# Performance work log

Hardware: AMD Instinct MI355X
Metric: run time of the kernel (lower is better)

## Reference

```python
import jax, jax.numpy as jnp
import numpy as np

B, L, C, R = 4, 2048, 16, 16
A_SCALE = 0.05  # keep spectral radius of transition matrices < 1 over L=2048 steps


def setup_inputs() -> dict:
    key = jax.random.key(0)
    k1, k2 = jax.random.split(key)
    A = jax.random.normal(k1, (B, L, C, R, R), dtype=jnp.float32) * A_SCALE
    X = jax.random.normal(k2, (B, L, C, R, R), dtype=jnp.float32)
    return {"A": A, "X": X}


def reference(A, X):
    # Linear matrix recurrence: Y_t = A_t @ Y_{t-1} + X_t (Y_0 = X_0),
    # computed in log-depth via an associative scan over the time axis (L).
    # Combine rule matches the Triton scan_combine_matrix:
    #   a_new = a_curr @ a_prev;  x_new = a_curr @ x_prev + x_curr
    def combine(e1, e2):
        a1, x1 = e1  # earlier segment
        a2, x2 = e2  # later segment
        a = jnp.einsum('blcik,blckj->blcij', a2, a1)
        x = jnp.einsum('blcik,blckj->blcij', a2, x1) + x2
        return (a, x)

    _, Y = jax.lax.associative_scan(combine, (A, X), axis=1)
    return Y  # [B, L, C, R, R]
```

## Files before the change

### kernel.cpp

```cpp
#include <hip/hip_runtime.h>

constexpr int B = 4, L = 2048, C = 16, R = 16;
constexpr int M = R * R;
constexpr int G = 64;
constexpr int S = L / G;
constexpr int T = 4;

__device__ __forceinline__ long mat_off(int b, int l, int c) {
    return (((long)b * L + l) * C + c) * M;
}

__global__ __launch_bounds__(256) void pass1_chunk_agg(
    const float* __restrict__ A, const float* __restrict__ X,
    float* __restrict__ ws) {
    const int blk = blockIdx.x;
    const int g   = blk % G;
    const int bc  = blk / G;
    const int b   = bc / C, c = bc % C;
    const int tid = threadIdx.x;
    const int i = tid >> 4, j = tid & 15;

    __shared__ float sA[T][M];
    __shared__ float sX[T][M];
    __shared__ float aggA[M];
    __shared__ float aggX[M];

    aggA[tid] = (i == j) ? 1.0f : 0.0f;
    aggX[tid] = 0.0f;

    const int tm = tid >> 6;
    const int e4 = (tid & 63) << 2;

    for (int t0 = 0; t0 < S; t0 += T) {
        const int l = g * S + t0 + tm;
        const float4 va = *(const float4*)(A + mat_off(b, l, c) + e4);
        const float4 vx = *(const float4*)(X + mat_off(b, l, c) + e4);
        *(float4*)&sA[tm][e4] = va;
        *(float4*)&sX[tm][e4] = vx;
        __syncthreads();
        for (int s = 0; s < T; ++s) {
            float accA = 0.0f;
            float accX = sX[s][tid];
            #pragma unroll
            for (int k = 0; k < 16; ++k) {
                const float a = sA[s][(i << 4) + k];
                accA += a * aggA[(k << 4) + j];
                accX += a * aggX[(k << 4) + j];
            }
            __syncthreads();
            aggA[tid] = accA;
            aggX[tid] = accX;
            __syncthreads();
        }
    }
    float* slot = ws + (long)blk * (2 * M);
    slot[tid]     = aggA[tid];
    slot[M + tid] = aggX[tid];
}

__global__ __launch_bounds__(256) void pass2_scan(float* __restrict__ ws) {
    const int bc  = blockIdx.x;
    const int tid = threadIdx.x;
    const int i = tid >> 4, j = tid & 15;

    __shared__ float sAg[M];
    __shared__ float carry[M];
    carry[tid] = 0.0f;

    float* base = ws + (long)bc * G * (2 * M);
    for (int g = 0; g < G; ++g) {
        float* slot = base + (long)g * (2 * M);
        sAg[tid] = slot[tid];
        const float xg  = slot[M + tid];
        const float old = carry[tid];
        __syncthreads();
        float acc = xg;
        #pragma unroll
        for (int k = 0; k < 16; ++k)
            acc += sAg[(i << 4) + k] * carry[(k << 4) + j];
        slot[M + tid] = old;
        __syncthreads();
        carry[tid] = acc;
        __syncthreads();
    }
}

__global__ __launch_bounds__(256) void pass3_apply(
    const float* __restrict__ A, const float* __restrict__ X,
    const float* __restrict__ ws, float* __restrict__ out) {
    const int blk = blockIdx.x;
    const int g   = blk % G;
    const int bc  = blk / G;
    const int b   = bc / C, c = bc % C;
    const int tid = threadIdx.x;
    const int i = tid >> 4, j = tid & 15;

    __shared__ float sA[T][M];
    __shared__ float sX[T][M];
    __shared__ float Y[M];

    Y[tid] = ws[(long)blk * (2 * M) + M + tid];

    const int tm = tid >> 6;
    const int e4 = (tid & 63) << 2;

    for (int t0 = 0; t0 < S; t0 += T) {
        const int l = g * S + t0 + tm;
        const float4 va = *(const float4*)(A + mat_off(b, l, c) + e4);
        const float4 vx = *(const float4*)(X + mat_off(b, l, c) + e4);
        *(float4*)&sA[tm][e4] = va;
        *(float4*)&sX[tm][e4] = vx;
        __syncthreads();
        for (int s = 0; s < T; ++s) {
            float acc = sX[s][tid];
            #pragma unroll
            for (int k = 0; k < 16; ++k)
                acc += sA[s][(i << 4) + k] * Y[(k << 4) + j];
            __syncthreads();
            Y[tid] = acc;
            out[mat_off(b, g * S + t0 + s, c) + tid] = acc;
            __syncthreads();
        }
    }
}

extern "C" void kernel_launch(void* const* d_in, const int* in_sizes, int n_in,
                              void* d_out, int out_size, void* d_ws, size_t ws_size,
                              hipStream_t stream) {
    const float* A = (const float*)d_in[0];
    const float* X = (const float*)d_in[1];
    float* out = (float*)d_out;
    float* ws  = (float*)d_ws;

    pass1_chunk_agg<<<B * C * G, 256, 0, stream>>>(A, X, ws);
    pass2_scan<<<B * C, 256, 0, stream>>>(ws);
    pass3_apply<<<B * C * G, 256, 0, stream>>>(A, X, ws, out);
}
```

Before: 400.9 us.

## Rewrite scan passes as single-wavefront register-tiled 4x4 matmul kernels

All three passes are rewritten so that one 64-lane wavefront handles four chunks, with each lane computing a 4x4 register tile of the 16x16 products. Shared memory uses a padded, swizzled layout, A is double-buffered, and the next step's loads are prefetched into registers. This removes the __syncthreads barriers and the one-element-per-thread scalar LDS traffic. Pass2 keeps the carry in registers and prefetches the next aggregate. In exchange, register pressure rises and there are far fewer threads per block, which may limit latency hiding.

```diff
diff --git a/kernel.cpp b/kernel.cpp
--- a/kernel.cpp
+++ b/kernel.cpp
@@ -1,126 +1,300 @@
 #include <hip/hip_runtime.h>
 
-constexpr int B = 4, L = 2048, C = 16, R = 16;
-constexpr int M = R * R;
-constexpr int G = 64;
-constexpr int S = L / G;
-constexpr int T = 4;
-
-__device__ __forceinline__ long mat_off(int b, int l, int c) {
-    return (((long)b * L + l) * C + c) * M;
-}
-
-__global__ __launch_bounds__(256) void pass1_chunk_agg(
-    const float* __restrict__ A, const float* __restrict__ X,
-    float* __restrict__ ws) {
-    const int blk = blockIdx.x;
-    const int g   = blk % G;
-    const int bc  = blk / G;
-    const int b   = bc / C, c = bc % C;
-    const int tid = threadIdx.x;
-    const int i = tid >> 4, j = tid & 15;
-
-    __shared__ float sA[T][M];
-    __shared__ float sX[T][M];
-    __shared__ float aggA[M];
-    __shared__ float aggX[M];
-
-    aggA[tid] = (i == j) ? 1.0f : 0.0f;
-    aggX[tid] = 0.0f;
-
-    const int tm = tid >> 6;
-    const int e4 = (tid & 63) << 2;
-
-    for (int t0 = 0; t0 < S; t0 += T) {
-        const int l = g * S + t0 + tm;
-        const float4 va = *(const float4*)(A + mat_off(b, l, c) + e4);
-        const float4 vx = *(const float4*)(X + mat_off(b, l, c) + e4);
-        *(float4*)&sA[tm][e4] = va;
-        *(float4*)&sX[tm][e4] = vx;
-        __syncthreads();
-        for (int s = 0; s < T; ++s) {
-            float accA = 0.0f;
-            float accX = sX[s][tid];
-            #pragma unroll
-            for (int k = 0; k < 16; ++k) {
-                const float a = sA[s][(i << 4) + k];
-                accA += a * aggA[(k << 4) + j];
-                accX += a * aggX[(k << 4) + j];
+
+constexpr int B_ = 4, L_ = 2048, C_ = 16;
+constexpr int G_ = 64;
+constexpr int S_ = 32;
+constexpr int RS = 272;
+
+__device__ __forceinline__ int swz(int row, int kb) {
+    return row * 16 + (((kb + (row >> 2)) & 3) << 2);
+}
+
+__global__ __launch_bounds__(64) void pass1(const float* __restrict__ A,
+                                            const float* __restrict__ X,
+                                            float* __restrict__ ws) {
+    const int lane = threadIdx.x & 63;
+    const int d    = lane >> 4;
+    const int p    = lane & 15;
+    const int i0   = (p >> 2) << 2;
+    const int j0   = (p & 3) << 2;
+    const int i0g  = p >> 2;
+    const int j0g  = p & 3;
+
+    long base4[4];
+#pragma unroll
+    for (int dd = 0; dd < 4; ++dd) {
+        const int ch = blockIdx.x * 4 + dd;
+        const int bc = ch >> 6, g = ch & 63;
+        base4[dd] = ((((long)(bc >> 4)) * L_ + (long)g * S_) * C_ + (bc & 15)) * 256;
+    }
+    const long lstep  = (long)C_ * 256;
+    const long mybase = base4[d];
+
+    __shared__ float sA[2][4 * RS];
+    __shared__ float aT[4 * RS];
+    __shared__ float xT[4 * RS];
+
+    const int soff = swz(lane >> 2, lane & 3);
+
+    float4 preA[4];
+#pragma unroll
+    for (int dd = 0; dd < 4; ++dd) preA[dd] = *(const float4*)(A + base4[dd] + 4 * lane);
+#pragma unroll
+    for (int dd = 0; dd < 4; ++dd) *(float4*)&sA[0][dd * RS + soff] = preA[dd];
+
+    float4 preX[4];
+#pragma unroll
+    for (int r = 0; r < 4; ++r)
+        preX[r] = *(const float4*)(X + mybase + (i0 + r) * 16 + j0);
+
+#pragma unroll
+    for (int dd = 0; dd < 4; ++dd)
+        preA[dd] = *(const float4*)(A + base4[dd] + lstep + 4 * lane);
+
+    float nA[4][4], nX[4][4];
+#pragma unroll
+    for (int r = 0; r < 4; ++r) {
+        float av[4], xv[4];
+        *(float4*)av = *(const float4*)&sA[0][d * RS + swz(i0 + r, j0g)];
+        *(float4*)xv = preX[r];
+#pragma unroll
+        for (int cc = 0; cc < 4; ++cc) { nA[cc][r] = av[cc]; nX[cc][r] = xv[cc]; }
+    }
+
+    int cur = 0;
+    for (int t = 1; t < S_; ++t) {
+        cur ^= 1;
+#pragma unroll
+        for (int dd = 0; dd < 4; ++dd) *(float4*)&sA[cur][dd * RS + soff] = preA[dd];
+#pragma unroll
+        for (int cc = 0; cc < 4; ++cc) {
+            *(float4*)&aT[d * RS + swz(j0 + cc, i0g)] =
+                make_float4(nA[cc][0], nA[cc][1], nA[cc][2], nA[cc][3]);
+            *(float4*)&xT[d * RS + swz(j0 + cc, i0g)] =
+                make_float4(nX[cc][0], nX[cc][1], nX[cc][2], nX[cc][3]);
+        }
+        float xt[4][4];
+#pragma unroll
+        for (int r = 0; r < 4; ++r) {
+            float xv[4]; *(float4*)xv = preX[r];
+#pragma unroll
+            for (int cc = 0; cc < 4; ++cc) xt[cc][r] = xv[cc];
+        }
+        const int tn = (t + 1 < S_) ? (t + 1) : (S_ - 1);
+#pragma unroll
+        for (int dd = 0; dd < 4; ++dd)
+            preA[dd] = *(const float4*)(A + base4[dd] + (long)tn * lstep + 4 * lane);
+#pragma unroll
+        for (int r = 0; r < 4; ++r)
+            preX[r] = *(const float4*)(X + mybase + (long)tn * lstep + (i0 + r) * 16 + j0);
+
+        float rA[4][4], rX[4][4];
+#pragma unroll
+        for (int cc = 0; cc < 4; ++cc)
+#pragma unroll
+            for (int r = 0; r < 4; ++r) { rA[cc][r] = 0.f; rX[cc][r] = xt[cc][r]; }
+#pragma unroll
+        for (int kb = 0; kb < 4; ++kb) {
+            float ar[4][4], ta[4][4], tx[4][4];
+#pragma unroll
+            for (int r = 0; r < 4; ++r)
+                *(float4*)ar[r] = *(const float4*)&sA[cur][d * RS + swz(i0 + r, kb)];
+#pragma unroll
+            for (int cc = 0; cc < 4; ++cc) {
+                *(float4*)ta[cc] = *(const float4*)&aT[d * RS + swz(j0 + cc, kb)];
+                *(float4*)tx[cc] = *(const float4*)&xT[d * RS + swz(j0 + cc, kb)];
             }
-            __syncthreads();
-            aggA[tid] = accA;
-            aggX[tid] = accX;
-            __syncthreads();
-        }
-    }
-    float* slot = ws + (long)blk * (2 * M);
-    slot[tid]     = aggA[tid];
-    slot[M + tid] = aggX[tid];
-}
-
-__global__ __launch_bounds__(256) void pass2_scan(float* __restrict__ ws) {
-    const int bc  = blockIdx.x;
-    const int tid = threadIdx.x;
-    const int i = tid >> 4, j = tid & 15;
-
-    __shared__ float sAg[M];
-    __shared__ float carry[M];
-    carry[tid] = 0.0f;
-
-    float* base = ws + (long)bc * G * (2 * M);
-    for (int g = 0; g < G; ++g) {
-        float* slot = base + (long)g * (2 * M);
-        sAg[tid] = slot[tid];
-        const float xg  = slot[M + tid];
-        const float old = carry[tid];
-        __syncthreads();
-        float acc = xg;
-        #pragma unroll
-        for (int k = 0; k < 16; ++k)
-            acc += sAg[(i << 4) + k] * carry[(k << 4) + j];
-        slot[M + tid] = old;
-        __syncthreads();
-        carry[tid] = acc;
-        __syncthreads();
-    }
-}
-
-__global__ __launch_bounds__(256) void pass3_apply(
-    const float* __restrict__ A, const float* __restrict__ X,
-    const float* __restrict__ ws, float* __restrict__ out) {
-    const int blk = blockIdx.x;
-    const int g   = blk % G;
-    const int bc  = blk / G;
-    const int b   = bc / C, c = bc % C;
-    const int tid = threadIdx.x;
-    const int i = tid >> 4, j = tid & 15;
-
-    __shared__ float sA[T][M];
-    __shared__ float sX[T][M];
-    __shared__ float Y[M];
-
-    Y[tid] = ws[(long)blk * (2 * M) + M + tid];
-
-    const int tm = tid >> 6;
-    const int e4 = (tid & 63) << 2;
-
-    for (int t0 = 0; t0 < S; t0 += T) {
-        const int l = g * S + t0 + tm;
-        const float4 va = *(const float4*)(A + mat_off(b, l, c) + e4);
-        const float4 vx = *(const float4*)(X + mat_off(b, l, c) + e4);
-        *(float4*)&sA[tm][e4] = va;
-        *(float4*)&sX[tm][e4] = vx;
-        __syncthreads();
-        for (int s = 0; s < T; ++s) {
-            float acc = sX[s][tid];
-            #pragma unroll
-            for (int k = 0; k < 16; ++k)
-                acc += sA[s][(i << 4) + k] * Y[(k << 4) + j];
-            __syncthreads();
-            Y[tid] = acc;
-            out[mat_off(b, g * S + t0 + s, c) + tid] = acc;
-            __syncthreads();
-        }
+#pragma unroll
+            for (int cc = 0; cc < 4; ++cc)
+#pragma unroll
+                for (int r = 0; r < 4; ++r)
+#pragma unroll
+                    for (int q = 0; q < 4; ++q) {
+                        rA[cc][r] += ar[r][q] * ta[cc][q];
+                        rX[cc][r] += ar[r][q] * tx[cc][q];
+                    }
+        }
+#pragma unroll
+        for (int cc = 0; cc < 4; ++cc)
+#pragma unroll
+            for (int r = 0; r < 4; ++r) { nA[cc][r] = rA[cc][r]; nX[cc][r] = rX[cc][r]; }
+    }
+
+    const int chunk = blockIdx.x * 4 + d;
+    float* slot = ws + (long)chunk * 512;
+#pragma unroll
+    for (int r = 0; r < 4; ++r) {
+        *(float4*)(slot + (i0 + r) * 16 + j0) =
+            make_float4(nA[0][r], nA[1][r], nA[2][r], nA[3][r]);
+        *(float4*)(slot + 256 + (i0 + r) * 16 + j0) =
+            make_float4(nX[0][r], nX[1][r], nX[2][r], nX[3][r]);
+    }
+}
+
+__global__ __launch_bounds__(64) void pass2(float* __restrict__ ws) {
+    const int lane = threadIdx.x & 63;
+    const int r0 = (lane >> 3) << 1;
+    const int c0 = (lane & 7) << 1;
+    float* base = ws + (long)blockIdx.x * G_ * 512;
+
+    __shared__ float cT[16 * 20];
+
+    float cy[2][2] = {{0.f, 0.f}, {0.f, 0.f}};
+
+    float4 Ag[2][4]; float2 Xg[2];
+#pragma unroll
+    for (int rr = 0; rr < 2; ++rr) {
+#pragma unroll
+        for (int kb = 0; kb < 4; ++kb)
+            Ag[rr][kb] = *(const float4*)(base + (r0 + rr) * 16 + kb * 4);
+        Xg[rr] = *(const float2*)(base + 256 + (r0 + rr) * 16 + c0);
+    }
+
+    for (int g = 0; g < G_; ++g) {
+        float* slot = base + (long)g * 512;
+        const int gn = (g + 1 < G_) ? (g + 1) : g;
+        float* nslot = base + (long)gn * 512;
+        float4 nAg[2][4]; float2 nXg[2];
+#pragma unroll
+        for (int rr = 0; rr < 2; ++rr) {
+#pragma unroll
+            for (int kb = 0; kb < 4; ++kb)
+                nAg[rr][kb] = *(const float4*)(nslot + (r0 + rr) * 16 + kb * 4);
+            nXg[rr] = *(const float2*)(nslot + 256 + (r0 + rr) * 16 + c0);
+        }
+#pragma unroll
+        for (int rr = 0; rr < 2; ++rr)
+            *(float2*)(slot + 256 + (r0 + rr) * 16 + c0) = make_float2(cy[rr][0], cy[rr][1]);
+#pragma unroll
+        for (int cc = 0; cc < 2; ++cc) {
+            cT[(c0 + cc) * 20 + r0 + 0] = cy[0][cc];
+            cT[(c0 + cc) * 20 + r0 + 1] = cy[1][cc];
+        }
+        float nc[2][2] = {{Xg[0].x, Xg[0].y}, {Xg[1].x, Xg[1].y}};
+#pragma unroll
+        for (int kb = 0; kb < 4; ++kb) {
+            float t0[4], t1[4], a0[4], a1[4];
+            *(float4*)t0 = *(const float4*)&cT[(c0 + 0) * 20 + kb * 4];
+            *(float4*)t1 = *(const float4*)&cT[(c0 + 1) * 20 + kb * 4];
+            *(float4*)a0 = Ag[0][kb];
+            *(float4*)a1 = Ag[1][kb];
+#pragma unroll
+            for (int q = 0; q < 4; ++q) {
+                nc[0][0] += a0[q] * t0[q];
+                nc[0][1] += a0[q] * t1[q];
+                nc[1][0] += a1[q] * t0[q];
+                nc[1][1] += a1[q] * t1[q];
+            }
+        }
+#pragma unroll
+        for (int rr = 0; rr < 2; ++rr) {
+            cy[rr][0] = nc[rr][0]; cy[rr][1] = nc[rr][1];
+            Xg[rr] = nXg[rr];
+#pragma unroll
+            for (int kb = 0; kb < 4; ++kb) Ag[rr][kb] = nAg[rr][kb];
+        }
+    }
+}
+
+__global__ __launch_bounds__(64) void pass3(const float* __restrict__ A,
+                                            const float* __restrict__ X,
+                                            const float* __restrict__ ws,
+                                            float* __restrict__ out) {
+    const int lane = threadIdx.x & 63;
+    const int d    = lane >> 4;
+    const int p    = lane & 15;
+    const int i0   = (p >> 2) << 2;
+    const int j0   = (p & 3) << 2;
+    const int i0g  = p >> 2;
+
+    long base4[4];
+#pragma unroll
+    for (int dd = 0; dd < 4; ++dd) {
+        const int ch = blockIdx.x * 4 + dd;
+        const int bc = ch >> 6, g = ch & 63;
+        base4[dd] = ((((long)(bc >> 4)) * L_ + (long)g * S_) * C_ + (bc & 15)) * 256;
+    }
+    const long lstep  = (long)C_ * 256;
+    const long mybase = base4[d];
+
+    __shared__ float sA[2][4 * RS];
+    __shared__ float yT[4 * RS];
+
+    const int soff = swz(lane >> 2, lane & 3);
+
+    const int chunk = blockIdx.x * 4 + d;
+    const float* cslot = ws + (long)chunk * 512 + 256;
+    float nY[4][4];
+#pragma unroll
+    for (int r = 0; r < 4; ++r) {
+        float cv[4]; *(float4*)cv = *(const float4*)(cslot + (i0 + r) * 16 + j0);
+#pragma unroll
+        for (int cc = 0; cc < 4; ++cc) nY[cc][r] = cv[cc];
+    }
+
+    float4 preA[4], preX[4];
+#pragma unroll
+    for (int dd = 0; dd < 4; ++dd) preA[dd] = *(const float4*)(A + base4[dd] + 4 * lane);
+#pragma unroll
+    for (int r = 0; r < 4; ++r)
+        preX[r] = *(const float4*)(X + mybase + (i0 + r) * 16 + j0);
+
+    int cur = 1;
+    for (int t = 0; t < S_; ++t) {
+        cur ^= 1;
+#pragma unroll
+        for (int dd = 0; dd < 4; ++dd) *(float4*)&sA[cur][dd * RS + soff] = preA[dd];
+#pragma unroll
+        for (int cc = 0; cc < 4; ++cc)
+            *(float4*)&yT[d * RS + swz(j0 + cc, i0g)] =
+                make_float4(nY[cc][0], nY[cc][1], nY[cc][2], nY[cc][3]);
+        float xt[4][4];
+#pragma unroll
+        for (int r = 0; r < 4; ++r) {
+            float xv[4]; *(float4*)xv = preX[r];
+#pragma unroll
+            for (int cc = 0; cc < 4; ++cc) xt[cc][r] = xv[cc];
+        }
+        const int tn = (t + 1 < S_) ? (t + 1) : (S_ - 1);
+#pragma unroll
+        for (int dd = 0; dd < 4; ++dd)
+            preA[dd] = *(const float4*)(A + base4[dd] + (long)tn * lstep + 4 * lane);
+#pragma unroll
+        for (int r = 0; r < 4; ++r)
+            preX[r] = *(const float4*)(X + mybase + (long)tn * lstep + (i0 + r) * 16 + j0);
+
+        float rY[4][4];
+#pragma unroll
+        for (int cc = 0; cc < 4; ++cc)
+#pragma unroll
+            for (int r = 0; r < 4; ++r) rY[cc][r] = xt[cc][r];
+#pragma unroll
+        for (int kb = 0; kb < 4; ++kb) {
+            float ar[4][4], ty[4][4];
+#pragma unroll
+            for (int r = 0; r < 4; ++r)
+                *(float4*)ar[r] = *(const float4*)&sA[cur][d * RS + swz(i0 + r, kb)];
+#pragma unroll
+            for (int cc = 0; cc < 4; ++cc)
+                *(float4*)ty[cc] = *(const float4*)&yT[d * RS + swz(j0 + cc, kb)];
+#pragma unroll
+            for (int cc = 0; cc < 4; ++cc)
+#pragma unroll
+                for (int r = 0; r < 4; ++r)
+#pragma unroll
+                    for (int q = 0; q < 4; ++q)
+                        rY[cc][r] += ar[r][q] * ty[cc][q];
+        }
+#pragma unroll
+        for (int cc = 0; cc < 4; ++cc)
+#pragma unroll
+            for (int r = 0; r < 4; ++r) nY[cc][r] = rY[cc][r];
+
+#pragma unroll
+        for (int r = 0; r < 4; ++r)
+            *(float4*)(out + mybase + (long)t * lstep + (i0 + r) * 16 + j0) =
+                make_float4(nY[0][r], nY[1][r], nY[2][r], nY[3][r]);
     }
 }
 
@@ -132,7 +306,7 @@
     float* out = (float*)d_out;
     float* ws  = (float*)d_ws;
 
-    pass1_chunk_agg<<<B * C * G, 256, 0, stream>>>(A, X, ws);
-    pass2_scan<<<B * C, 256, 0, stream>>>(ws);
-    pass3_apply<<<B * C * G, 256, 0, stream>>>(A, X, ws, out);
-}
+    pass1<<<1024, 64, 0, stream>>>(A, X, ws);
+    pass2<<<64, 64, 0, stream>>>(ws);
+    pass3<<<1024, 64, 0, stream>>>(A, X, ws, out);
+}
```

New measurement: 608.4 us. +51.8%, slower.
